# Kernel optimization log

Measured on AMD Instinct MI355X. Metric: run time of the kernel, lower is better.

Reference implementation:

```python
import jax, jax.numpy as jnp
import numpy as np
from jax import lax

RADIUS = 0.2
MAX_SAMPLES = 64
B, C, N = 16, 3, 2048


def setup_inputs() -> dict:
    key = jax.random.key(0)
    # point clouds uniform in unit cube, layout (B, 3, N) as in pointnet repos
    pcs = jax.random.uniform(key, (B, C, N), dtype=jnp.float32)
    return {"pcs": pcs}


def reference(pcs):
    # Self ball-point query: for every point i, gather up to MAX_SAMPLES indices j
    # with ||p_i - p_j||^2 < RADIUS^2 (in ascending index order, the standard CUDA
    # ball-query scan order); unused slots are padded with the first found index.
    # The query point itself (dist 0) is always within radius, so every row has
    # at least one valid neighbor.
    x = jnp.swapaxes(pcs, 1, 2)                    # (B, N, 3)
    d2 = jnp.sum((x[:, :, None, :] - x[:, None, :, :]) ** 2, axis=-1)  # (B, N, N)
    within = d2 < (RADIUS * RADIUS)
    n = x.shape[1]
    idx = jnp.arange(n, dtype=jnp.int32)
    # key = j if within radius else n (sentinel); smallest K keys = first K neighbors
    keys = jnp.where(within, idx[None, None, :], n)  # (B, N, N) int32
    # top_k of negated keys -> K smallest keys, ascending after negation
    neg_topk, _ = lax.top_k(-keys, MAX_SAMPLES)      # (B, N, K)
    first_k = -neg_topk                              # ascending indices, sentinels last
    first = first_k[..., :1]                         # first valid neighbor (pad value)
    group_idx = jnp.where(first_k == n, first, first_k)
    return group_idx.astype(jnp.int64)
```

## Files before the change

kernel.cpp:

```cpp
#include <hip/hip_runtime.h>
#include <hip/hip_bf16.h>
#include <stdint.h>


#define B_DIM 16
#define N_PTS 2048
#define K_OUT 64
#define R2 0.04f
#define WAVES 16
#define BLOCK_T (WAVES * 64)
#define JPW (N_PTS / WAVES)
#define WPW (JPW / 32)
#define ROWPAD 65

typedef float v2f __attribute__((ext_vector_type(2)));

__global__ __launch_bounds__(BLOCK_T, 8) void ball_query_kernel(
    const float* __restrict__ pcs,
    int* __restrict__ out)
{
    __shared__ int rows[64 * ROWPAD];
    __shared__ int cntS[WAVES][64];
    __shared__ int qfS[WAVES][64];

    const int b    = blockIdx.x >> 5;
    const int qg   = blockIdx.x & 31;
    const int tid  = threadIdx.x;
    const int wave = __builtin_amdgcn_readfirstlane(tid >> 6);
    const int lane = tid & 63;

    const float* __restrict__ sx = pcs + (size_t)b * 3 * N_PTS;
    const float* __restrict__ sy = sx + N_PTS;
    const float* __restrict__ sz = sy + N_PTS;

    const int qi = qg * 64 + lane;
    const float nx = -sx[qi], ny = -sy[qi], nz = -sz[qi];
    const v2f nqx = {nx, nx}, nqy = {ny, ny}, nqz = {nz, nz};

    const int jbase = wave * JPW;
    int* const obase = out + (size_t)(b * N_PTS + qg * 64) * K_OUT;

    unsigned mask[WPW];
    #pragma unroll
    for (int t = 0; t < WPW; ++t) {
        unsigned m = 0;
        #pragma unroll
        for (int k = 30; k >= 0; k -= 2) {
            const int j = jbase + t * 32 + k;
            const v2f px = *(const v2f*)(sx + j);
            const v2f py = *(const v2f*)(sy + j);
            const v2f pz = *(const v2f*)(sz + j);
            v2f dx, dy, dz, xx, yy, zz, s0, d2;
            asm("v_pk_add_f32 %0, %1, %2" : "=v"(dx) : "s"(px), "v"(nqx));
            asm("v_pk_add_f32 %0, %1, %2" : "=v"(dy) : "s"(py), "v"(nqy));
            asm("v_pk_add_f32 %0, %1, %2" : "=v"(dz) : "s"(pz), "v"(nqz));
            asm("v_pk_mul_f32 %0, %1, %1" : "=v"(xx) : "v"(dx));
            asm("v_pk_mul_f32 %0, %1, %1" : "=v"(yy) : "v"(dy));
            asm("v_pk_mul_f32 %0, %1, %1" : "=v"(zz) : "v"(dz));
            asm("v_pk_add_f32 %0, %1, %2" : "=v"(s0) : "v"(xx), "v"(yy));
            asm("v_pk_add_f32 %0, %1, %2" : "=v"(d2) : "v"(s0), "v"(zz));
            m = m + m + (unsigned)(d2.y < R2);
            m = m + m + (unsigned)(d2.x < R2);
        }
        mask[t] = m;
    }

    int cnt = 0;
    #pragma unroll
    for (int t = 0; t < WPW; ++t) cnt += __builtin_popcount(mask[t]);
    int qf = -1;
    #pragma unroll
    for (int t = 0; t < WPW; ++t) {
        if (qf < 0 && mask[t] != 0u)
            qf = jbase + t * 32 + __builtin_ctz(mask[t]);
    }
    cntS[wave][lane] = cnt;
    qfS[wave][lane]  = qf;
    __syncthreads();

    int base = 0, tc = 0, gfirst = 0;
    #pragma unroll
    for (int w = 0; w < WAVES; ++w) {
        const int c = cntS[w][lane];
        const int f = qfS[w][lane];
        if (w < wave) base += c;
        gfirst = (tc == 0 && c > 0) ? f : gfirst;
        tc += c;
    }

    int slot = base;
    for (int t = 0; t < WPW; ++t) {
        unsigned m = mask[t];
        while (m != 0u && slot < K_OUT) {
            const int k = (int)__builtin_ctz(m);
            rows[lane * ROWPAD + slot] = jbase + t * 32 + k;
            m &= m - 1u;
            ++slot;
        }
    }

    #pragma unroll
    for (int s0i = 0; s0i < K_OUT / WAVES; ++s0i) {
        const int s = wave * (K_OUT / WAVES) + s0i;
        if (s >= tc) rows[lane * ROWPAD + s] = gfirst;
    }
    __syncthreads();

    #pragma unroll
    for (int it = 0; it < (64 * K_OUT) / BLOCK_T; ++it) {
        const int idx = it * BLOCK_T + tid;
        const int r = idx >> 6;
        const int c = idx & 63;
        obase[idx] = rows[r * ROWPAD + c];
    }
}

extern "C" void kernel_launch(void* const* d_in, const int* in_sizes, int n_in,
                              void* d_out, int out_size, void* d_ws, size_t ws_size,
                              hipStream_t stream) {
    const float* pcs = (const float*)d_in[0];
    int* out = (int*)d_out;
    const int grid = B_DIM * 32;
    ball_query_kernel<<<grid, BLOCK_T, 0, stream>>>(pcs, out);
}
```

Measured before the change: 78.46 us.

## Transpose distance loop: lanes own candidates, broadcast queries, build masks via ballot

Each lane now holds two candidate points in registers and the wave loops over the 64 query points, which are loaded as vectors and broadcast as scalars. Per-query neighbor bitmasks come from wave ballots, and the lane matching each query keeps its 128-bit mask. This replaces per-iteration scalar loads of candidate coordinates with vector loads of query coordinates, at the cost of a ballot and lane select per query. The resulting mask bit order matches the old per-lane layout, since lane l covers j=jbase+l and j=jbase+64+l.

```diff
diff --git a/kernel.cpp b/kernel.cpp
--- a/kernel.cpp
+++ b/kernel.cpp
@@ -1,5 +1,4 @@
 #include <hip/hip_runtime.h>
-#include <hip/hip_bf16.h>
 #include <stdint.h>
 
 
@@ -14,6 +13,7 @@
 #define ROWPAD 65
 
 typedef float v2f __attribute__((ext_vector_type(2)));
+typedef float f32x8 __attribute__((ext_vector_type(8)));
 
 __global__ __launch_bounds__(BLOCK_T, 8) void ball_query_kernel(
     const float* __restrict__ pcs,
@@ -33,37 +33,53 @@
     const float* __restrict__ sy = sx + N_PTS;
     const float* __restrict__ sz = sy + N_PTS;
 
-    const int qi = qg * 64 + lane;
-    const float nx = -sx[qi], ny = -sy[qi], nz = -sz[qi];
-    const v2f nqx = {nx, nx}, nqy = {ny, ny}, nqz = {nz, nz};
+    const int jbase = wave * JPW;
+    const int qb    = qg * 64;
+    int* const obase = out + (size_t)(b * N_PTS + qb) * K_OUT;
 
-    const int jbase = wave * JPW;
-    int* const obase = out + (size_t)(b * N_PTS + qg * 64) * K_OUT;
+    v2f px, py, pz;
+    px.x = sx[jbase + lane]; px.y = sx[jbase + 64 + lane];
+    py.x = sy[jbase + lane]; py.y = sy[jbase + 64 + lane];
+    pz.x = sz[jbase + lane]; pz.y = sz[jbase + 64 + lane];
 
-    unsigned mask[WPW];
+    unsigned w0 = 0, w1 = 0, w2 = 0, w3 = 0;
+
     #pragma unroll
-    for (int t = 0; t < WPW; ++t) {
-        unsigned m = 0;
+    for (int c = 0; c < 8; ++c) {
+        const f32x8 qxv = *(const f32x8*)(sx + qb + c * 8);
+        const f32x8 qyv = *(const f32x8*)(sy + qb + c * 8);
+        const f32x8 qzv = *(const f32x8*)(sz + qb + c * 8);
         #pragma unroll
-        for (int k = 30; k >= 0; k -= 2) {
-            const int j = jbase + t * 32 + k;
-            const v2f px = *(const v2f*)(sx + j);
-            const v2f py = *(const v2f*)(sy + j);
-            const v2f pz = *(const v2f*)(sz + j);
+        for (int s = 0; s < 8; ++s) {
+            const int q = c * 8 + s;
+            const unsigned bx = __float_as_uint(qxv[s]) ^ 0x80000000u;
+            const unsigned by = __float_as_uint(qyv[s]) ^ 0x80000000u;
+            const unsigned bz = __float_as_uint(qzv[s]) ^ 0x80000000u;
+            v2f nX, nY, nZ;
+            nX.x = nX.y = __uint_as_float(bx);
+            nY.x = nY.y = __uint_as_float(by);
+            nZ.x = nZ.y = __uint_as_float(bz);
             v2f dx, dy, dz, xx, yy, zz, s0, d2;
-            asm("v_pk_add_f32 %0, %1, %2" : "=v"(dx) : "s"(px), "v"(nqx));
-            asm("v_pk_add_f32 %0, %1, %2" : "=v"(dy) : "s"(py), "v"(nqy));
-            asm("v_pk_add_f32 %0, %1, %2" : "=v"(dz) : "s"(pz), "v"(nqz));
+            asm("v_pk_add_f32 %0, %1, %2" : "=v"(dx) : "s"(nX), "v"(px));
+            asm("v_pk_add_f32 %0, %1, %2" : "=v"(dy) : "s"(nY), "v"(py));
+            asm("v_pk_add_f32 %0, %1, %2" : "=v"(dz) : "s"(nZ), "v"(pz));
             asm("v_pk_mul_f32 %0, %1, %1" : "=v"(xx) : "v"(dx));
             asm("v_pk_mul_f32 %0, %1, %1" : "=v"(yy) : "v"(dy));
             asm("v_pk_mul_f32 %0, %1, %1" : "=v"(zz) : "v"(dz));
             asm("v_pk_add_f32 %0, %1, %2" : "=v"(s0) : "v"(xx), "v"(yy));
             asm("v_pk_add_f32 %0, %1, %2" : "=v"(d2) : "v"(s0), "v"(zz));
-            m = m + m + (unsigned)(d2.y < R2);
-            m = m + m + (unsigned)(d2.x < R2);
+            const unsigned long long b0 = __ballot(d2.x < R2);
+            const unsigned long long b1 = __ballot(d2.y < R2);
+            if (lane == q) {
+                w0 = (unsigned)b0;
+                w1 = (unsigned)(b0 >> 32);
+                w2 = (unsigned)b1;
+                w3 = (unsigned)(b1 >> 32);
+            }
         }
-        mask[t] = m;
     }
+
+    unsigned mask[WPW] = { w0, w1, w2, w3 };
 
     int cnt = 0;
     #pragma unroll
```

New measurement: 73.77 us, median of 2. 1.06x faster.
